# Optimization experiments

Measured on AMD Instinct MI355X. Metric: run time of the kernel, lower is better.

Reference implementation:

```python
import jax, jax.numpy as jnp
import numpy as np

B, N, T, F, H = 64, 307, 64, 3, 64
LN_EPS = 1e-5


def _layernorm(h, g, b):
    mu = h.mean(-1, keepdims=True)
    var = ((h - mu) ** 2).mean(-1, keepdims=True)
    return (h - mu) * jax.lax.rsqrt(var + LN_EPS) * g + b


def setup_inputs() -> dict:
    key = jax.random.key(0)
    ks = jax.random.split(key, 14)
    x_seq = jax.random.normal(ks[0], (B, N, T, F), dtype=jnp.float32)
    obs_mask = (jax.random.uniform(ks[1], (B, N, 1, 1)) < 0.7).astype(jnp.float32)
    # symmetric degree-normalized Gaussian-kernel adjacency [N, N]
    d = jax.random.uniform(ks[2], (N, N))
    adj = jnp.exp(-(d ** 2))
    adj = 0.5 * (adj + adj.T)
    deg = adj.sum(1)
    dinv = jnp.where(deg > 0, deg ** -0.5, 0.0)
    A = (adj * dinv[:, None] * dinv[None, :]).astype(jnp.float32)

    def lin(k, fan_in, shape):
        return (jax.random.normal(k, shape, dtype=jnp.float32) / np.sqrt(fan_in)).astype(jnp.float32)

    return {
        "x_seq": x_seq, "obs_mask": obs_mask, "A": A,
        "W_enc": lin(ks[3], F, (F, H)), "b_enc": jnp.zeros((H,), jnp.float32),
        "W_gc1": lin(ks[4], H, (H, H)),
        "W_gc2": lin(ks[5], H, (H, H)),
        "ln_g": jnp.ones((H,), jnp.float32), "ln_b": jnp.zeros((H,), jnp.float32),
        "W_obs": lin(ks[6], F, (F, H)), "b_obs": jnp.zeros((H,), jnp.float32),
        "W_gate": lin(ks[7], 2 * H, (2 * H, H)), "b_gate": jnp.zeros((H,), jnp.float32),
        "W_dec": lin(ks[8], H, (H, 1)), "b_dec": jnp.zeros((1,), jnp.float32),
    }


def reference(x_seq, obs_mask, A, W_enc, b_enc, W_gc1, W_gc2, ln_g, ln_b,
              W_obs, b_obs, W_gate, b_gate, W_dec, b_dec):
    mask = obs_mask[:, :, 0, :]                      # [B, N, 1]
    z0 = x_seq[:, :, 0, :] @ W_enc + b_enc           # [B, N, H]
    xs = jnp.moveaxis(x_seq[:, :, 1:, :], 2, 0)      # [T-1, B, N, F]

    def step(z, x_new):
        pred = z @ W_dec + b_dec                     # decoder before update
        # Euler step: z + ode_func(z), ode_func(x) = x + LN(tanh(gc2(tanh(gc1(x)))))
        h = jnp.tanh(jnp.einsum('nm,bmd->bnd', A, z) @ W_gc1)
        h = jnp.tanh(jnp.einsum('nm,bmd->bnd', A, h) @ W_gc2)
        delta = _layernorm(h, ln_g, ln_b)
        z = z + (z + delta)
        # gated assimilation of the new observation
        z_obs = x_new @ W_obs + b_obs
        gate = jax.nn.sigmoid(jnp.concatenate([z, z_obs], axis=-1) @ W_gate + b_gate)
        z = z + gate * (z_obs - z) * mask
        return z, pred

    z_final, preds = jax.lax.scan(step, z0, xs)      # preds: [T-1, B, N, 1]
    pred_last = z_final @ W_dec + b_dec
    preds = jnp.concatenate([preds, pred_last[None]], axis=0)  # [T, B, N, 1]
    return jnp.moveaxis(preds, 0, 2)                 # [B, N, T, 1]
```

## Files before the change

### kernel.cpp

```cpp
#include <hip/hip_runtime.h>

typedef unsigned short u16;
typedef __attribute__((ext_vector_type(8))) short short8;
typedef __attribute__((ext_vector_type(4))) float f32x4;
typedef __attribute__((ext_vector_type(4))) int i32x4;
typedef __attribute__((ext_vector_type(4))) unsigned short u16x4;

#define NN 307
#define NP 320
#define TT 64
#define LDP 76
#define LWS 68
#define LNEPS 1e-5f

__device__ __forceinline__ u16 f2bf(float f) {
  union { float f; unsigned u; } v; v.f = f;
  unsigned r = (v.u + 0x7FFFu + ((v.u >> 16) & 1u)) >> 16;
  return (u16)r;
}
__device__ __forceinline__ float bf2f(u16 h) {
  union { unsigned u; float f; } v; v.u = ((unsigned)h) << 16;
  return v.f;
}
__device__ __forceinline__ void split3(float v, u16 &h, u16 &m, u16 &l) {
  h = f2bf(v);
  float r1 = v - bf2f(h);
  m = f2bf(r1);
  float r2 = r1 - bf2f(m);
  l = f2bf(r2);
}

#define MFMA(a, b, c) __builtin_amdgcn_mfma_f32_16x16x32_bf16((a), (b), (c), 0, 0, 0)

__device__ __forceinline__ void gemm_block(
    const u16* __restrict__ A_hi, const u16* __restrict__ A_md, const u16* __restrict__ A_lo,
    const u16* __restrict__ X_hi, const u16* __restrict__ X_md, const u16* __restrict__ X_lo,
    int c0, int n0, int tid, f32x4 acc[2][2])
{
  const int w = tid >> 6, l = tid & 63, lr = l & 15, lg = l >> 4;
  const int wr = w >> 1, wc = w & 1;
  const size_t xr0 = (size_t)(c0 + wr * 32 + lr) * NP;
  const size_t xr1 = xr0 + (size_t)16 * NP;
  const size_t ar0 = (size_t)(n0 + wc * 32 + lr) * NP;
  const size_t ar1 = ar0 + (size_t)16 * NP;
  for (int kk = 0; kk < 10; ++kk) {
    const int ko = kk * 32 + lg * 8;
    short8 xh[2], xm[2], xl[2], ah[2], am[2], al[2];
    xh[0] = *(const short8*)&X_hi[xr0 + ko];
    xm[0] = *(const short8*)&X_md[xr0 + ko];
    xl[0] = *(const short8*)&X_lo[xr0 + ko];
    xh[1] = *(const short8*)&X_hi[xr1 + ko];
    xm[1] = *(const short8*)&X_md[xr1 + ko];
    xl[1] = *(const short8*)&X_lo[xr1 + ko];
    ah[0] = *(const short8*)&A_hi[ar0 + ko];
    am[0] = *(const short8*)&A_md[ar0 + ko];
    al[0] = *(const short8*)&A_lo[ar0 + ko];
    ah[1] = *(const short8*)&A_hi[ar1 + ko];
    am[1] = *(const short8*)&A_md[ar1 + ko];
    al[1] = *(const short8*)&A_lo[ar1 + ko];
#pragma unroll
    for (int fr = 0; fr < 2; ++fr) {
#pragma unroll
      for (int fc = 0; fc < 2; ++fc) {
        f32x4 a = acc[fr][fc];
        a = MFMA(xh[fr], ah[fc], a);
        a = MFMA(xh[fr], am[fc], a);
        a = MFMA(xm[fr], ah[fc], a);
        a = MFMA(xh[fr], al[fc], a);
        a = MFMA(xl[fr], ah[fc], a);
        a = MFMA(xm[fr], am[fc], a);
        acc[fr][fc] = a;
      }
    }
  }
}

__device__ __forceinline__ void store_G(f32x4 acc[2][2], float* ldsG, int tid) {
  const int w = tid >> 6, l = tid & 63, lr = l & 15, lg = l >> 4;
  const int wr = w >> 1, wc = w & 1;
#pragma unroll
  for (int fr = 0; fr < 2; ++fr) {
#pragma unroll
    for (int fc = 0; fc < 2; ++fc) {
      const int nn = wc * 32 + fc * 16 + lr;
      const int quad = (8 * wr + 4 * fr + lg) ^ (nn & 15);
      *(f32x4*)&ldsG[nn * LDP + quad * 4] = acc[fr][fc];
    }
  }
}

__device__ __forceinline__ void mat64(const float* ldsG, const float* ldsW,
                                      int nq, int dq, float o[4][4]) {
#pragma unroll
  for (int j = 0; j < 4; ++j)
#pragma unroll
    for (int c = 0; c < 4; ++c) o[j][c] = 0.f;
  for (int d4 = 0; d4 < 16; ++d4) {
    f32x4 gr[4], wv[4];
#pragma unroll
    for (int j = 0; j < 4; ++j) {
      const int nl = nq * 4 + j;
      gr[j] = *(const f32x4*)&ldsG[nl * LDP + ((d4 ^ (nl & 15)) << 2)];
    }
#pragma unroll
    for (int m = 0; m < 4; ++m)
      wv[m] = *(const f32x4*)&ldsW[(d4 * 4 + m) * LWS + dq * 4];
#pragma unroll
    for (int j = 0; j < 4; ++j) {
#pragma unroll
      for (int m = 0; m < 4; ++m) {
        const float zz = gr[j][m];
#pragma unroll
        for (int c = 0; c < 4; ++c) o[j][c] += zz * wv[m][c];
      }
    }
  }
}

__device__ __forceinline__ void stage_W(const float* __restrict__ W, float* ldsW, int tid) {
  const int d = tid >> 2, ch = (tid & 3) << 4;
#pragma unroll
  for (int j = 0; j < 16; ++j)
    ldsW[d * LWS + ch + j] = W[d * 64 + ch + j];
}

__global__ __launch_bounds__(256) void k_prep(
    const float* __restrict__ A, const float* __restrict__ W_obs,
    const float* __restrict__ b_obs, const float* __restrict__ W_gate,
    u16* __restrict__ A_hi, u16* __restrict__ A_md, u16* __restrict__ A_lo,
    float* __restrict__ Wf, float* __restrict__ bfold)
{
  if (blockIdx.x < 400) {
    const int e = blockIdx.x * 256 + threadIdx.x;
    const int r = e / NP, c = e - r * NP;
    const float a = (r < NN && c < NN) ? A[r * NN + c] : 0.f;
    u16 h, m, l;
    split3(a, h, m, l);
    A_hi[e] = h; A_md[e] = m; A_lo[e] = l;
  } else if (threadIdx.x < 64) {
    const int dp = threadIdx.x;
    float s0 = 0.f, s1 = 0.f, s2 = 0.f, sb = 0.f;
    for (int d = 0; d < 64; ++d) {
      const float wg = W_gate[(64 + d) * 64 + dp];
      s0 += W_obs[d] * wg;
      s1 += W_obs[64 + d] * wg;
      s2 += W_obs[128 + d] * wg;
      sb += b_obs[d] * wg;
    }
    Wf[dp] = s0; Wf[64 + dp] = s1; Wf[128 + dp] = s2; bfold[dp] = sb;
  }
}

__global__ __launch_bounds__(256) void k_init(
    const float* __restrict__ x_seq, const float* __restrict__ W_enc,
    const float* __restrict__ b_enc, const float* __restrict__ W_dec,
    const float* __restrict__ b_dec,
    float* __restrict__ zf,
    u16* __restrict__ Z_hi, u16* __restrict__ Z_md, u16* __restrict__ Z_lo,
    float* __restrict__ out)
{
  const int b = blockIdx.x, n0 = blockIdx.y * 64;
  const int tid = threadIdx.x;
  __shared__ float xs[256], we[192], be[64], wd[64];
  __shared__ float ldsR[16 * 64];
  if (tid < 64) {
    const int n = n0 + tid;
    float x0 = 0.f, x1 = 0.f, x2 = 0.f;
    if (n < NN) {
      const size_t xo = ((size_t)(b * NN + n) * TT + 0) * 3;
      x0 = x_seq[xo]; x1 = x_seq[xo + 1]; x2 = x_seq[xo + 2];
    }
    xs[tid * 4] = x0; xs[tid * 4 + 1] = x1; xs[tid * 4 + 2] = x2; xs[tid * 4 + 3] = 0.f;
    be[tid] = b_enc[tid]; wd[tid] = W_dec[tid];
  } else {
    const int e = tid - 64;
    if (e < 192) we[e] = W_enc[e];
  }
  __syncthreads();
  const int nq = tid & 15, dq = tid >> 4;
  float zn[4][4];
  float p[4] = {0.f, 0.f, 0.f, 0.f};
#pragma unroll
  for (int j = 0; j < 4; ++j) {
    const int nl = nq * 4 + j;
    const bool v = (n0 + nl) < NN;
    const float x0 = xs[nl * 4], x1 = xs[nl * 4 + 1], x2 = xs[nl * 4 + 2];
#pragma unroll
    for (int c = 0; c < 4; ++c) {
      const int d = dq * 4 + c;
      float z = x0 * we[d] + x1 * we[64 + d] + x2 * we[128 + d] + be[d];
      z = v ? z : 0.f;
      zn[j][c] = z;
      p[j] += z * wd[d];
    }
  }
#pragma unroll
  for (int c = 0; c < 4; ++c) {
    const int d = dq * 4 + c;
    const size_t off = (size_t)(b * 64 + d) * NP + n0 + nq * 4;
    f32x4 vf = { zn[0][c], zn[1][c], zn[2][c], zn[3][c] };
    *(f32x4*)&zf[off] = vf;
    u16x4 vh, vm, vl;
#pragma unroll
    for (int j = 0; j < 4; ++j) {
      u16 hh, mm2, ll;
      split3(zn[j][c], hh, mm2, ll);
      vh[j] = hh; vm[j] = mm2; vl[j] = ll;
    }
    *(u16x4*)&Z_hi[off] = vh;
    *(u16x4*)&Z_md[off] = vm;
    *(u16x4*)&Z_lo[off] = vl;
  }
#pragma unroll
  for (int j = 0; j < 4; ++j) ldsR[dq * 64 + nq * 4 + j] = p[j];
  __syncthreads();
  if (tid < 64) {
    const int n = n0 + tid;
    if (n < NN) {
      float s = 0.f;
#pragma unroll
      for (int q = 0; q < 16; ++q) s += ldsR[q * 64 + tid];
      out[(size_t)(b * NN + n) * TT + 0] = s + b_dec[0];
    }
  }
}

__global__ __launch_bounds__(256) void k_step1(
    const u16* __restrict__ A_hi, const u16* __restrict__ A_md, const u16* __restrict__ A_lo,
    const u16* __restrict__ X_hi, const u16* __restrict__ X_md, const u16* __restrict__ X_lo,
    const float* __restrict__ W_gc1,
    u16* __restrict__ O_hi, u16* __restrict__ O_md, u16* __restrict__ O_lo)
{
  const int b = blockIdx.x, n0 = blockIdx.y * 64, c0 = b * 64;
  const int tid = threadIdx.x;
  __shared__ __align__(16) float ldsG[64 * LDP];
  __shared__ __align__(16) float ldsW[64 * LWS];
  stage_W(W_gc1, ldsW, tid);
  f32x4 acc[2][2];
  acc[0][0] = 0.f; acc[0][1] = 0.f; acc[1][0] = 0.f; acc[1][1] = 0.f;
  gemm_block(A_hi, A_md, A_lo, X_hi, X_md, X_lo, c0, n0, tid, acc);
  store_G(acc, ldsG, tid);
  __syncthreads();
  const int nq = tid & 15, dq = tid >> 4;
  float mx[4][4];
  mat64(ldsG, ldsW, nq, dq, mx);
#pragma unroll
  for (int c = 0; c < 4; ++c) {
    u16x4 vh, vm, vl;
#pragma unroll
    for (int j = 0; j < 4; ++j) {
      const float v = tanhf(mx[j][c]);
      u16 hh, mm2, ll;
      split3(v, hh, mm2, ll);
      vh[j] = hh; vm[j] = mm2; vl[j] = ll;
    }
    const size_t off = (size_t)(c0 + dq * 4 + c) * NP + n0 + nq * 4;
    *(u16x4*)&O_hi[off] = vh;
    *(u16x4*)&O_md[off] = vm;
    *(u16x4*)&O_lo[off] = vl;
  }
}

__global__ __launch_bounds__(256) void k_step2(
    const u16* __restrict__ A_hi, const u16* __restrict__ A_md, const u16* __restrict__ A_lo,
    const u16* __restrict__ X_hi, const u16* __restrict__ X_md, const u16* __restrict__ X_lo,
    const float* __restrict__ W_gc2,
    const float* __restrict__ x_seq, const float* __restrict__ obs_mask,
    const float* __restrict__ W_gate, const float* __restrict__ b_gate,
    const float* __restrict__ ln_g, const float* __restrict__ ln_b,
    const float* __restrict__ W_obs, const float* __restrict__ b_obs,
    const float* __restrict__ Wf, const float* __restrict__ bfold,
    const float* __restrict__ W_dec, const float* __restrict__ b_dec,
    float* __restrict__ zf,
    u16* __restrict__ Z_hi, u16* __restrict__ Z_md, u16* __restrict__ Z_lo,
    float* __restrict__ out, int t)
{
  const int b = blockIdx.x, n0 = blockIdx.y * 64, c0 = b * 64;
  const int tid = threadIdx.x;
  __shared__ __align__(16) float ldsG[64 * LDP];
  __shared__ __align__(16) float ldsW[64 * LWS];
  __shared__ __align__(16) float ldsWg[64 * LWS];
  __shared__ float ldsR[16 * 64];
  __shared__ float ldsMu[64], ldsRs[64];
  __shared__ float sLng[64], sLnb[64], sWd[64], sBg[64], sBo[64], sBf[64], sMask[64];
  __shared__ float sWo[192], sWfl[192], sXv[256];

  stage_W(W_gc2, ldsW, tid);
  stage_W(W_gate, ldsWg, tid);
  if (tid < 64) {
    sLng[tid] = ln_g[tid]; sLnb[tid] = ln_b[tid]; sWd[tid] = W_dec[tid];
    sBg[tid] = b_gate[tid]; sBo[tid] = b_obs[tid]; sBf[tid] = bfold[tid];
    const int n = n0 + tid;
    sMask[tid] = (n < NN) ? obs_mask[b * NN + n] : 0.f;
    float x0 = 0.f, x1 = 0.f, x2 = 0.f;
    if (n < NN) {
      const size_t xo = ((size_t)(b * NN + n) * TT + (t + 1)) * 3;
      x0 = x_seq[xo]; x1 = x_seq[xo + 1]; x2 = x_seq[xo + 2];
    }
    sXv[tid * 4] = x0; sXv[tid * 4 + 1] = x1; sXv[tid * 4 + 2] = x2; sXv[tid * 4 + 3] = 0.f;
  } else {
    const int e = tid - 64;
    if (e < 192) { sWo[e] = W_obs[e]; sWfl[e] = Wf[e]; }
  }

  f32x4 acc[2][2];
  acc[0][0] = 0.f; acc[0][1] = 0.f; acc[1][0] = 0.f; acc[1][1] = 0.f;
  gemm_block(A_hi, A_md, A_lo, X_hi, X_md, X_lo, c0, n0, tid, acc);
  store_G(acc, ldsG, tid);
  __syncthreads();

  const int nq = tid & 15, dq = tid >> 4;
  float mx[4][4];
  mat64(ldsG, ldsW, nq, dq, mx);
  float h2[4][4];
#pragma unroll
  for (int j = 0; j < 4; ++j)
#pragma unroll
    for (int c = 0; c < 4; ++c) h2[j][c] = tanhf(mx[j][c]);

#pragma unroll
  for (int j = 0; j < 4; ++j)
    ldsR[dq * 64 + nq * 4 + j] = h2[j][0] + h2[j][1] + h2[j][2] + h2[j][3];
  __syncthreads();
  if (tid < 64) {
    float s = 0.f;
#pragma unroll
    for (int q = 0; q < 16; ++q) s += ldsR[q * 64 + tid];
    ldsMu[tid] = s * (1.f / 64.f);
  }
  __syncthreads();
#pragma unroll
  for (int j = 0; j < 4; ++j) {
    const float mu = ldsMu[nq * 4 + j];
    float qq = 0.f;
#pragma unroll
    for (int c = 0; c < 4; ++c) { const float dd = h2[j][c] - mu; qq += dd * dd; }
    ldsR[dq * 64 + nq * 4 + j] = qq;
  }
  __syncthreads();
  if (tid < 64) {
    float s = 0.f;
#pragma unroll
    for (int q = 0; q < 16; ++q) s += ldsR[q * 64 + tid];
    ldsRs[tid] = rsqrtf(s * (1.f / 64.f) + LNEPS);
  }
  __syncthreads();

  f32x4 zoldv[4];
#pragma unroll
  for (int c = 0; c < 4; ++c)
    zoldv[c] = *(const f32x4*)&zf[(size_t)(c0 + dq * 4 + c) * NP + n0 + nq * 4];
  float zpr[4][4];
#pragma unroll
  for (int j = 0; j < 4; ++j) {
    const int nl = nq * 4 + j;
    const float mu = ldsMu[nl], rs = ldsRs[nl];
#pragma unroll
    for (int c = 0; c < 4; ++c) {
      const int dpp = dq * 4 + c;
      const float delta = (h2[j][c] - mu) * rs * sLng[dpp] + sLnb[dpp];
      zpr[j][c] = 2.f * zoldv[c][j] + delta;
    }
    f32x4 zrow = { zpr[j][0], zpr[j][1], zpr[j][2], zpr[j][3] };
    *(f32x4*)&ldsG[nl * LDP + ((dq ^ (nl & 15)) << 2)] = zrow;
  }
  __syncthreads();

  float ps[4][4];
  mat64(ldsG, ldsWg, nq, dq, ps);

  float znew[4][4];
  float p[4] = {0.f, 0.f, 0.f, 0.f};
#pragma unroll
  for (int j = 0; j < 4; ++j) {
    const int nl = nq * 4 + j;
    const bool valid = (n0 + nl) < NN;
    const float x0 = sXv[nl * 4], x1 = sXv[nl * 4 + 1], x2 = sXv[nl * 4 + 2];
    const float mk = sMask[nl];
#pragma unroll
    for (int c = 0; c < 4; ++c) {
      const int dpp = dq * 4 + c;
      const float presig = ps[j][c] + sBg[dpp] + sBf[dpp]
          + x0 * sWfl[dpp] + x1 * sWfl[64 + dpp] + x2 * sWfl[128 + dpp];
      const float gate = 1.f / (1.f + expf(-presig));
      const float zobs = x0 * sWo[dpp] + x1 * sWo[64 + dpp] + x2 * sWo[128 + dpp] + sBo[dpp];
      float zn2 = zpr[j][c] + gate * (zobs - zpr[j][c]) * mk;
      zn2 = valid ? zn2 : 0.f;
      znew[j][c] = zn2;
      p[j] += zn2 * sWd[dpp];
    }
  }
#pragma unroll
  for (int c = 0; c < 4; ++c) {
    const size_t off = (size_t)(c0 + dq * 4 + c) * NP + n0 + nq * 4;
    f32x4 vf = { znew[0][c], znew[1][c], znew[2][c], znew[3][c] };
    *(f32x4*)&zf[off] = vf;
    u16x4 vh, vm, vl;
#pragma unroll
    for (int j = 0; j < 4; ++j) {
      u16 hh, mm2, ll;
      split3(znew[j][c], hh, mm2, ll);
      vh[j] = hh; vm[j] = mm2; vl[j] = ll;
    }
    *(u16x4*)&Z_hi[off] = vh;
    *(u16x4*)&Z_md[off] = vm;
    *(u16x4*)&Z_lo[off] = vl;
  }
#pragma unroll
  for (int j = 0; j < 4; ++j) ldsR[dq * 64 + nq * 4 + j] = p[j];
  __syncthreads();
  if (tid < 64) {
    const int n = n0 + tid;
    if (n < NN) {
      float s = 0.f;
#pragma unroll
      for (int q = 0; q < 16; ++q) s += ldsR[q * 64 + tid];
      out[(size_t)(b * NN + n) * TT + (t + 1)] = s + b_dec[0];
    }
  }
}

extern "C" void kernel_launch(void* const* d_in, const int* in_sizes, int n_in,
                              void* d_out, int out_size, void* d_ws, size_t ws_size,
                              hipStream_t stream) {
  const float* x_seq  = (const float*)d_in[0];
  const float* obs    = (const float*)d_in[1];
  const float* A      = (const float*)d_in[2];
  const float* W_enc  = (const float*)d_in[3];
  const float* b_enc  = (const float*)d_in[4];
  const float* W_gc1  = (const float*)d_in[5];
  const float* W_gc2  = (const float*)d_in[6];
  const float* ln_g   = (const float*)d_in[7];
  const float* ln_b   = (const float*)d_in[8];
  const float* W_obs  = (const float*)d_in[9];
  const float* b_obs  = (const float*)d_in[10];
  const float* W_gate = (const float*)d_in[11];
  const float* b_gate = (const float*)d_in[12];
  const float* W_dec  = (const float*)d_in[13];
  const float* b_dec  = (const float*)d_in[14];
  float* out = (float*)d_out;

  char* p = (char*)d_ws;
  u16* A_hi = (u16*)p; p += (size_t)NP * NP * 2;
  u16* A_md = (u16*)p; p += (size_t)NP * NP * 2;
  u16* A_lo = (u16*)p; p += (size_t)NP * NP * 2;
  u16* z_hi = (u16*)p; p += (size_t)4096 * NP * 2;
  u16* z_md = (u16*)p; p += (size_t)4096 * NP * 2;
  u16* z_lo = (u16*)p; p += (size_t)4096 * NP * 2;
  u16* h_hi = (u16*)p; p += (size_t)4096 * NP * 2;
  u16* h_md = (u16*)p; p += (size_t)4096 * NP * 2;
  u16* h_lo = (u16*)p; p += (size_t)4096 * NP * 2;
  float* zf = (float*)p; p += (size_t)4096 * NP * 4;
  float* Wf = (float*)p; p += 256 * 4;
  float* bfold = (float*)p; p += 64 * 4;

  dim3 grid(64, 5);
  k_prep<<<401, 256, 0, stream>>>(A, W_obs, b_obs, W_gate, A_hi, A_md, A_lo, Wf, bfold);
  k_init<<<grid, 256, 0, stream>>>(x_seq, W_enc, b_enc, W_dec, b_dec,
                                   zf, z_hi, z_md, z_lo, out);
  for (int t = 0; t < 63; ++t) {
    k_step1<<<grid, 256, 0, stream>>>(A_hi, A_md, A_lo, z_hi, z_md, z_lo, W_gc1,
                                      h_hi, h_md, h_lo);
    k_step2<<<grid, 256, 0, stream>>>(A_hi, A_md, A_lo, h_hi, h_md, h_lo, W_gc2,
                                      x_seq, obs, W_gate, b_gate, ln_g, ln_b,
                                      W_obs, b_obs, Wf, bfold, W_dec, b_dec,
                                      zf, z_hi, z_md, z_lo, out, t);
  }
  (void)in_sizes; (void)n_in; (void)out_size; (void)ws_size;
}
```

Baseline: 12.76 ms.

## Fuse all time steps into one persistent kernel per batch element

Replaces the 127 per-step kernel launches (init plus two per step) with one persistent kernel of 64 blocks, one per batch, that loops over all 63 time steps internally. It keeps the fp32 state z in registers instead of a global buffer, and uses wave shuffles instead of LDS reductions for layernorm and decoder sums. This removes launch overhead and the global round-trips of z. The cost is that only 64 blocks occupy the GPU, far fewer than the CU count, so each block now carries a full 320x64 GEMM per stage. The H and Z split buffers still pass through global memory between stages, and their new per-element scalar stores are uncoalesced.

```diff
diff --git a/kernel.cpp b/kernel.cpp
--- a/kernel.cpp
+++ b/kernel.cpp
@@ -3,14 +3,12 @@
 typedef unsigned short u16;
 typedef __attribute__((ext_vector_type(8))) short short8;
 typedef __attribute__((ext_vector_type(4))) float f32x4;
-typedef __attribute__((ext_vector_type(4))) int i32x4;
-typedef __attribute__((ext_vector_type(4))) unsigned short u16x4;
 
 #define NN 307
 #define NP 320
 #define TT 64
-#define LDP 76
-#define LWS 68
+#define NB 64
+#define LDP 68
 #define LNEPS 1e-5f
 
 __device__ __forceinline__ u16 f2bf(float f) {
@@ -31,98 +29,6 @@
 }
 
 #define MFMA(a, b, c) __builtin_amdgcn_mfma_f32_16x16x32_bf16((a), (b), (c), 0, 0, 0)
-
-__device__ __forceinline__ void gemm_block(
-    const u16* __restrict__ A_hi, const u16* __restrict__ A_md, const u16* __restrict__ A_lo,
-    const u16* __restrict__ X_hi, const u16* __restrict__ X_md, const u16* __restrict__ X_lo,
-    int c0, int n0, int tid, f32x4 acc[2][2])
-{
-  const int w = tid >> 6, l = tid & 63, lr = l & 15, lg = l >> 4;
-  const int wr = w >> 1, wc = w & 1;
-  const size_t xr0 = (size_t)(c0 + wr * 32 + lr) * NP;
-  const size_t xr1 = xr0 + (size_t)16 * NP;
-  const size_t ar0 = (size_t)(n0 + wc * 32 + lr) * NP;
-  const size_t ar1 = ar0 + (size_t)16 * NP;
-  for (int kk = 0; kk < 10; ++kk) {
-    const int ko = kk * 32 + lg * 8;
-    short8 xh[2], xm[2], xl[2], ah[2], am[2], al[2];
-    xh[0] = *(const short8*)&X_hi[xr0 + ko];
-    xm[0] = *(const short8*)&X_md[xr0 + ko];
-    xl[0] = *(const short8*)&X_lo[xr0 + ko];
-    xh[1] = *(const short8*)&X_hi[xr1 + ko];
-    xm[1] = *(const short8*)&X_md[xr1 + ko];
-    xl[1] = *(const short8*)&X_lo[xr1 + ko];
-    ah[0] = *(const short8*)&A_hi[ar0 + ko];
-    am[0] = *(const short8*)&A_md[ar0 + ko];
-    al[0] = *(const short8*)&A_lo[ar0 + ko];
-    ah[1] = *(const short8*)&A_hi[ar1 + ko];
-    am[1] = *(const short8*)&A_md[ar1 + ko];
-    al[1] = *(const short8*)&A_lo[ar1 + ko];
-#pragma unroll
-    for (int fr = 0; fr < 2; ++fr) {
-#pragma unroll
-      for (int fc = 0; fc < 2; ++fc) {
-        f32x4 a = acc[fr][fc];
-        a = MFMA(xh[fr], ah[fc], a);
-        a = MFMA(xh[fr], am[fc], a);
-        a = MFMA(xm[fr], ah[fc], a);
-        a = MFMA(xh[fr], al[fc], a);
-        a = MFMA(xl[fr], ah[fc], a);
-        a = MFMA(xm[fr], am[fc], a);
-        acc[fr][fc] = a;
-      }
-    }
-  }
-}
-
-__device__ __forceinline__ void store_G(f32x4 acc[2][2], float* ldsG, int tid) {
-  const int w = tid >> 6, l = tid & 63, lr = l & 15, lg = l >> 4;
-  const int wr = w >> 1, wc = w & 1;
-#pragma unroll
-  for (int fr = 0; fr < 2; ++fr) {
-#pragma unroll
-    for (int fc = 0; fc < 2; ++fc) {
-      const int nn = wc * 32 + fc * 16 + lr;
-      const int quad = (8 * wr + 4 * fr + lg) ^ (nn & 15);
-      *(f32x4*)&ldsG[nn * LDP + quad * 4] = acc[fr][fc];
-    }
-  }
-}
-
-__device__ __forceinline__ void mat64(const float* ldsG, const float* ldsW,
-                                      int nq, int dq, float o[4][4]) {
-#pragma unroll
-  for (int j = 0; j < 4; ++j)
-#pragma unroll
-    for (int c = 0; c < 4; ++c) o[j][c] = 0.f;
-  for (int d4 = 0; d4 < 16; ++d4) {
-    f32x4 gr[4], wv[4];
-#pragma unroll
-    for (int j = 0; j < 4; ++j) {
-      const int nl = nq * 4 + j;
-      gr[j] = *(const f32x4*)&ldsG[nl * LDP + ((d4 ^ (nl & 15)) << 2)];
-    }
-#pragma unroll
-    for (int m = 0; m < 4; ++m)
-      wv[m] = *(const f32x4*)&ldsW[(d4 * 4 + m) * LWS + dq * 4];
-#pragma unroll
-    for (int j = 0; j < 4; ++j) {
-#pragma unroll
-      for (int m = 0; m < 4; ++m) {
-        const float zz = gr[j][m];
-#pragma unroll
-        for (int c = 0; c < 4; ++c) o[j][c] += zz * wv[m][c];
-      }
-    }
-  }
-}
-
-__device__ __forceinline__ void stage_W(const float* __restrict__ W, float* ldsW, int tid) {
-  const int d = tid >> 2, ch = (tid & 3) << 4;
-#pragma unroll
-  for (int j = 0; j < 16; ++j)
-    ldsW[d * LWS + ch + j] = W[d * 64 + ch + j];
-}
 
 __global__ __launch_bounds__(256) void k_prep(
     const float* __restrict__ A, const float* __restrict__ W_obs,
@@ -151,272 +57,241 @@
   }
 }
 
-__global__ __launch_bounds__(256) void k_init(
-    const float* __restrict__ x_seq, const float* __restrict__ W_enc,
-    const float* __restrict__ b_enc, const float* __restrict__ W_dec,
-    const float* __restrict__ b_dec,
-    float* __restrict__ zf,
+__device__ __forceinline__ void gemm_stage(
+    const u16* __restrict__ Xh, const u16* __restrict__ Xm, const u16* __restrict__ Xl,
+    const u16* __restrict__ Ah, const u16* __restrict__ Am, const u16* __restrict__ Al,
+    int b, int cr, int g160, int lr, int lg, float* ldsG)
+{
+  const size_t xbase = (size_t)(b * 64 + cr * 16 + lr) * NP;
+  f32x4 acc[10];
+#pragma unroll
+  for (int i = 0; i < 10; ++i) acc[i] = (f32x4){0.f, 0.f, 0.f, 0.f};
+  unsigned abase[10];
+#pragma unroll
+  for (int i = 0; i < 10; ++i) abase[i] = (unsigned)((g160 + i * 16 + lr) * NP);
+
+  for (int kk = 0; kk < 10; ++kk) {
+    const int ko = kk * 32 + lg * 8;
+    const short8 xh = *(const short8*)&Xh[xbase + ko];
+    const short8 xm = *(const short8*)&Xm[xbase + ko];
+    const short8 xl = *(const short8*)&Xl[xbase + ko];
+#pragma unroll
+    for (int i = 0; i < 10; ++i) {
+      const short8 ah = *(const short8*)&Ah[abase[i] + ko];
+      const short8 am = *(const short8*)&Am[abase[i] + ko];
+      const short8 al = *(const short8*)&Al[abase[i] + ko];
+      f32x4 a = acc[i];
+      a = MFMA(xh, ah, a);
+      a = MFMA(xh, am, a);
+      a = MFMA(xm, ah, a);
+      a = MFMA(xh, al, a);
+      a = MFMA(xl, ah, a);
+      a = MFMA(xm, am, a);
+      acc[i] = a;
+    }
+  }
+#pragma unroll
+  for (int i = 0; i < 10; ++i) {
+    const int n = g160 + i * 16 + lr;
+    const int q = cr * 4 + lg;
+    *(f32x4*)&ldsG[n * LDP + ((q ^ (n & 15)) << 2)] = acc[i];
+  }
+}
+
+__device__ __forceinline__ void mat64b(const float* __restrict__ ldsG,
+                                       const float* __restrict__ ldsW,
+                                       int nset, int dq, float o[10][4])
+{
+#pragma unroll
+  for (int i = 0; i < 10; ++i)
+#pragma unroll
+    for (int c = 0; c < 4; ++c) o[i][c] = 0.f;
+  const int nq15 = nset & 15;
+  for (int d4 = 0; d4 < 16; ++d4) {
+    f32x4 wv[4];
+#pragma unroll
+    for (int m = 0; m < 4; ++m)
+      wv[m] = *(const f32x4*)&ldsW[(d4 * 4 + m) * 64 + dq * 4];
+#pragma unroll
+    for (int i = 0; i < 10; ++i) {
+      const f32x4 gr = *(const f32x4*)&ldsG[(nset + 32 * i) * LDP + ((d4 ^ nq15) << 2)];
+#pragma unroll
+      for (int m = 0; m < 4; ++m) {
+        const float g = gr[m];
+#pragma unroll
+        for (int c = 0; c < 4; ++c) o[i][c] += g * wv[m][c];
+      }
+    }
+  }
+}
+
+__global__ __launch_bounds__(512, 1) void k_main(
+    const float* __restrict__ x_seq, const float* __restrict__ obs_mask,
+    const float* __restrict__ W_enc, const float* __restrict__ b_enc,
+    const float* __restrict__ ln_g, const float* __restrict__ ln_b,
+    const float* __restrict__ W_obs, const float* __restrict__ b_obs,
+    const float* __restrict__ W_gate, const float* __restrict__ b_gate,
+    const float* __restrict__ W_dec, const float* __restrict__ b_dec,
+    const float* __restrict__ W_gc1, const float* __restrict__ W_gc2,
+    const float* __restrict__ Wf, const float* __restrict__ bfold,
+    const u16* __restrict__ A_hi, const u16* __restrict__ A_md, const u16* __restrict__ A_lo,
     u16* __restrict__ Z_hi, u16* __restrict__ Z_md, u16* __restrict__ Z_lo,
+    u16* __restrict__ H_hi, u16* __restrict__ H_md, u16* __restrict__ H_lo,
     float* __restrict__ out)
 {
-  const int b = blockIdx.x, n0 = blockIdx.y * 64;
+  const int b = blockIdx.x;
   const int tid = threadIdx.x;
-  __shared__ float xs[256], we[192], be[64], wd[64];
-  __shared__ float ldsR[16 * 64];
-  if (tid < 64) {
-    const int n = n0 + tid;
+  const int w = tid >> 6, l = tid & 63, lr = l & 15, lg = l >> 4;
+  const int dq = tid & 15, nset = tid >> 4;
+  const int cr = w & 3, g160 = (w >> 2) * 160;
+
+  __shared__ __align__(16) float ldsG[NP * LDP];
+  __shared__ __align__(16) float ldsW1[64 * 64];
+  __shared__ __align__(16) float ldsW2[64 * 64];
+  __shared__ __align__(16) float ldsWg[64 * 64];
+  __shared__ float sXv[NP * 4];
+  __shared__ float sMask[NP];
+  __shared__ float sWo[192], sWfl[192], sWe[192];
+  __shared__ float sBe[64], sLng[64], sLnb[64], sWd[64], sBg[64], sBo[64], sBf[64];
+
+#pragma unroll
+  for (int j = 0; j < 8; ++j) {
+    ldsW1[tid * 8 + j] = W_gc1[tid * 8 + j];
+    ldsW2[tid * 8 + j] = W_gc2[tid * 8 + j];
+    ldsWg[tid * 8 + j] = W_gate[tid * 8 + j];
+  }
+  if (tid < 192) { sWo[tid] = W_obs[tid]; sWfl[tid] = Wf[tid]; sWe[tid] = W_enc[tid]; }
+  else if (tid < 256) {
+    const int d = tid - 192;
+    sBe[d] = b_enc[d]; sLng[d] = ln_g[d]; sLnb[d] = ln_b[d]; sWd[d] = W_dec[d];
+    sBg[d] = b_gate[d]; sBo[d] = b_obs[d]; sBf[d] = bfold[d];
+  }
+  if (tid < NP) {
+    const int n = tid;
+    sMask[n] = (n < NN) ? obs_mask[b * NN + n] : 0.f;
     float x0 = 0.f, x1 = 0.f, x2 = 0.f;
     if (n < NN) {
-      const size_t xo = ((size_t)(b * NN + n) * TT + 0) * 3;
+      const size_t xo = ((size_t)(b * NN + n) * TT) * 3;
       x0 = x_seq[xo]; x1 = x_seq[xo + 1]; x2 = x_seq[xo + 2];
     }
-    xs[tid * 4] = x0; xs[tid * 4 + 1] = x1; xs[tid * 4 + 2] = x2; xs[tid * 4 + 3] = 0.f;
-    be[tid] = b_enc[tid]; wd[tid] = W_dec[tid];
-  } else {
-    const int e = tid - 64;
-    if (e < 192) we[e] = W_enc[e];
-  }
+    sXv[n * 4] = x0; sXv[n * 4 + 1] = x1; sXv[n * 4 + 2] = x2; sXv[n * 4 + 3] = 0.f;
+  }
+  const float bdec = b_dec[0];
   __syncthreads();
-  const int nq = tid & 15, dq = tid >> 4;
-  float zn[4][4];
-  float p[4] = {0.f, 0.f, 0.f, 0.f};
-#pragma unroll
-  for (int j = 0; j < 4; ++j) {
-    const int nl = nq * 4 + j;
-    const bool v = (n0 + nl) < NN;
-    const float x0 = xs[nl * 4], x1 = xs[nl * 4 + 1], x2 = xs[nl * 4 + 2];
-#pragma unroll
-    for (int c = 0; c < 4; ++c) {
-      const int d = dq * 4 + c;
-      float z = x0 * we[d] + x1 * we[64 + d] + x2 * we[128 + d] + be[d];
-      z = v ? z : 0.f;
-      zn[j][c] = z;
-      p[j] += z * wd[d];
-    }
-  }
-#pragma unroll
-  for (int c = 0; c < 4; ++c) {
-    const int d = dq * 4 + c;
-    const size_t off = (size_t)(b * 64 + d) * NP + n0 + nq * 4;
-    f32x4 vf = { zn[0][c], zn[1][c], zn[2][c], zn[3][c] };
-    *(f32x4*)&zf[off] = vf;
-    u16x4 vh, vm, vl;
-#pragma unroll
-    for (int j = 0; j < 4; ++j) {
-      u16 hh, mm2, ll;
-      split3(zn[j][c], hh, mm2, ll);
-      vh[j] = hh; vm[j] = mm2; vl[j] = ll;
-    }
-    *(u16x4*)&Z_hi[off] = vh;
-    *(u16x4*)&Z_md[off] = vm;
-    *(u16x4*)&Z_lo[off] = vl;
-  }
-#pragma unroll
-  for (int j = 0; j < 4; ++j) ldsR[dq * 64 + nq * 4 + j] = p[j];
-  __syncthreads();
-  if (tid < 64) {
-    const int n = n0 + tid;
-    if (n < NN) {
-      float s = 0.f;
-#pragma unroll
-      for (int q = 0; q < 16; ++q) s += ldsR[q * 64 + tid];
-      out[(size_t)(b * NN + n) * TT + 0] = s + b_dec[0];
-    }
-  }
-}
-
-__global__ __launch_bounds__(256) void k_step1(
-    const u16* __restrict__ A_hi, const u16* __restrict__ A_md, const u16* __restrict__ A_lo,
-    const u16* __restrict__ X_hi, const u16* __restrict__ X_md, const u16* __restrict__ X_lo,
-    const float* __restrict__ W_gc1,
-    u16* __restrict__ O_hi, u16* __restrict__ O_md, u16* __restrict__ O_lo)
-{
-  const int b = blockIdx.x, n0 = blockIdx.y * 64, c0 = b * 64;
-  const int tid = threadIdx.x;
-  __shared__ __align__(16) float ldsG[64 * LDP];
-  __shared__ __align__(16) float ldsW[64 * LWS];
-  stage_W(W_gc1, ldsW, tid);
-  f32x4 acc[2][2];
-  acc[0][0] = 0.f; acc[0][1] = 0.f; acc[1][0] = 0.f; acc[1][1] = 0.f;
-  gemm_block(A_hi, A_md, A_lo, X_hi, X_md, X_lo, c0, n0, tid, acc);
-  store_G(acc, ldsG, tid);
-  __syncthreads();
-  const int nq = tid & 15, dq = tid >> 4;
-  float mx[4][4];
-  mat64(ldsG, ldsW, nq, dq, mx);
-#pragma unroll
-  for (int c = 0; c < 4; ++c) {
-    u16x4 vh, vm, vl;
-#pragma unroll
-    for (int j = 0; j < 4; ++j) {
-      const float v = tanhf(mx[j][c]);
-      u16 hh, mm2, ll;
-      split3(v, hh, mm2, ll);
-      vh[j] = hh; vm[j] = mm2; vl[j] = ll;
-    }
-    const size_t off = (size_t)(c0 + dq * 4 + c) * NP + n0 + nq * 4;
-    *(u16x4*)&O_hi[off] = vh;
-    *(u16x4*)&O_md[off] = vm;
-    *(u16x4*)&O_lo[off] = vl;
-  }
-}
-
-__global__ __launch_bounds__(256) void k_step2(
-    const u16* __restrict__ A_hi, const u16* __restrict__ A_md, const u16* __restrict__ A_lo,
-    const u16* __restrict__ X_hi, const u16* __restrict__ X_md, const u16* __restrict__ X_lo,
-    const float* __restrict__ W_gc2,
-    const float* __restrict__ x_seq, const float* __restrict__ obs_mask,
-    const float* __restrict__ W_gate, const float* __restrict__ b_gate,
-    const float* __restrict__ ln_g, const float* __restrict__ ln_b,
-    const float* __restrict__ W_obs, const float* __restrict__ b_obs,
-    const float* __restrict__ Wf, const float* __restrict__ bfold,
-    const float* __restrict__ W_dec, const float* __restrict__ b_dec,
-    float* __restrict__ zf,
-    u16* __restrict__ Z_hi, u16* __restrict__ Z_md, u16* __restrict__ Z_lo,
-    float* __restrict__ out, int t)
-{
-  const int b = blockIdx.x, n0 = blockIdx.y * 64, c0 = b * 64;
-  const int tid = threadIdx.x;
-  __shared__ __align__(16) float ldsG[64 * LDP];
-  __shared__ __align__(16) float ldsW[64 * LWS];
-  __shared__ __align__(16) float ldsWg[64 * LWS];
-  __shared__ float ldsR[16 * 64];
-  __shared__ float ldsMu[64], ldsRs[64];
-  __shared__ float sLng[64], sLnb[64], sWd[64], sBg[64], sBo[64], sBf[64], sMask[64];
-  __shared__ float sWo[192], sWfl[192], sXv[256];
-
-  stage_W(W_gc2, ldsW, tid);
-  stage_W(W_gate, ldsWg, tid);
-  if (tid < 64) {
-    sLng[tid] = ln_g[tid]; sLnb[tid] = ln_b[tid]; sWd[tid] = W_dec[tid];
-    sBg[tid] = b_gate[tid]; sBo[tid] = b_obs[tid]; sBf[tid] = bfold[tid];
-    const int n = n0 + tid;
-    sMask[tid] = (n < NN) ? obs_mask[b * NN + n] : 0.f;
-    float x0 = 0.f, x1 = 0.f, x2 = 0.f;
-    if (n < NN) {
-      const size_t xo = ((size_t)(b * NN + n) * TT + (t + 1)) * 3;
-      x0 = x_seq[xo]; x1 = x_seq[xo + 1]; x2 = x_seq[xo + 2];
-    }
-    sXv[tid * 4] = x0; sXv[tid * 4 + 1] = x1; sXv[tid * 4 + 2] = x2; sXv[tid * 4 + 3] = 0.f;
-  } else {
-    const int e = tid - 64;
-    if (e < 192) { sWo[e] = W_obs[e]; sWfl[e] = Wf[e]; }
-  }
-
-  f32x4 acc[2][2];
-  acc[0][0] = 0.f; acc[0][1] = 0.f; acc[1][0] = 0.f; acc[1][1] = 0.f;
-  gemm_block(A_hi, A_md, A_lo, X_hi, X_md, X_lo, c0, n0, tid, acc);
-  store_G(acc, ldsG, tid);
-  __syncthreads();
-
-  const int nq = tid & 15, dq = tid >> 4;
-  float mx[4][4];
-  mat64(ldsG, ldsW, nq, dq, mx);
-  float h2[4][4];
-#pragma unroll
-  for (int j = 0; j < 4; ++j)
-#pragma unroll
-    for (int c = 0; c < 4; ++c) h2[j][c] = tanhf(mx[j][c]);
-
-#pragma unroll
-  for (int j = 0; j < 4; ++j)
-    ldsR[dq * 64 + nq * 4 + j] = h2[j][0] + h2[j][1] + h2[j][2] + h2[j][3];
-  __syncthreads();
-  if (tid < 64) {
-    float s = 0.f;
-#pragma unroll
-    for (int q = 0; q < 16; ++q) s += ldsR[q * 64 + tid];
-    ldsMu[tid] = s * (1.f / 64.f);
-  }
-  __syncthreads();
-#pragma unroll
-  for (int j = 0; j < 4; ++j) {
-    const float mu = ldsMu[nq * 4 + j];
-    float qq = 0.f;
-#pragma unroll
-    for (int c = 0; c < 4; ++c) { const float dd = h2[j][c] - mu; qq += dd * dd; }
-    ldsR[dq * 64 + nq * 4 + j] = qq;
-  }
-  __syncthreads();
-  if (tid < 64) {
-    float s = 0.f;
-#pragma unroll
-    for (int q = 0; q < 16; ++q) s += ldsR[q * 64 + tid];
-    ldsRs[tid] = rsqrtf(s * (1.f / 64.f) + LNEPS);
-  }
-  __syncthreads();
-
-  f32x4 zoldv[4];
-#pragma unroll
-  for (int c = 0; c < 4; ++c)
-    zoldv[c] = *(const f32x4*)&zf[(size_t)(c0 + dq * 4 + c) * NP + n0 + nq * 4];
-  float zpr[4][4];
-#pragma unroll
-  for (int j = 0; j < 4; ++j) {
-    const int nl = nq * 4 + j;
-    const float mu = ldsMu[nl], rs = ldsRs[nl];
+
+  float zf[10][4];
+#pragma unroll
+  for (int i = 0; i < 10; ++i) {
+    const int n = nset + 32 * i;
+    const bool valid = n < NN;
+    const float x0 = sXv[n * 4], x1 = sXv[n * 4 + 1], x2 = sXv[n * 4 + 2];
+    float p = 0.f;
 #pragma unroll
     for (int c = 0; c < 4; ++c) {
       const int dpp = dq * 4 + c;
-      const float delta = (h2[j][c] - mu) * rs * sLng[dpp] + sLnb[dpp];
-      zpr[j][c] = 2.f * zoldv[c][j] + delta;
-    }
-    f32x4 zrow = { zpr[j][0], zpr[j][1], zpr[j][2], zpr[j][3] };
-    *(f32x4*)&ldsG[nl * LDP + ((dq ^ (nl & 15)) << 2)] = zrow;
+      float z = x0 * sWe[dpp] + x1 * sWe[64 + dpp] + x2 * sWe[128 + dpp] + sBe[dpp];
+      z = valid ? z : 0.f;
+      zf[i][c] = z;
+      u16 hh, mm, ll; split3(z, hh, mm, ll);
+      const size_t off = (size_t)(b * 64 + dpp) * NP + n;
+      Z_hi[off] = hh; Z_md[off] = mm; Z_lo[off] = ll;
+      p += z * sWd[dpp];
+    }
+#pragma unroll
+    for (int m = 1; m < 16; m <<= 1) p += __shfl_xor(p, m, 64);
+    if (dq == 0 && valid) out[(size_t)(b * NN + n) * TT] = p + bdec;
   }
   __syncthreads();
 
-  float ps[4][4];
-  mat64(ldsG, ldsWg, nq, dq, ps);
-
-  float znew[4][4];
-  float p[4] = {0.f, 0.f, 0.f, 0.f};
-#pragma unroll
-  for (int j = 0; j < 4; ++j) {
-    const int nl = nq * 4 + j;
-    const bool valid = (n0 + nl) < NN;
-    const float x0 = sXv[nl * 4], x1 = sXv[nl * 4 + 1], x2 = sXv[nl * 4 + 2];
-    const float mk = sMask[nl];
-#pragma unroll
-    for (int c = 0; c < 4; ++c) {
-      const int dpp = dq * 4 + c;
-      const float presig = ps[j][c] + sBg[dpp] + sBf[dpp]
-          + x0 * sWfl[dpp] + x1 * sWfl[64 + dpp] + x2 * sWfl[128 + dpp];
-      const float gate = 1.f / (1.f + expf(-presig));
-      const float zobs = x0 * sWo[dpp] + x1 * sWo[64 + dpp] + x2 * sWo[128 + dpp] + sBo[dpp];
-      float zn2 = zpr[j][c] + gate * (zobs - zpr[j][c]) * mk;
-      zn2 = valid ? zn2 : 0.f;
-      znew[j][c] = zn2;
-      p[j] += zn2 * sWd[dpp];
-    }
-  }
-#pragma unroll
-  for (int c = 0; c < 4; ++c) {
-    const size_t off = (size_t)(c0 + dq * 4 + c) * NP + n0 + nq * 4;
-    f32x4 vf = { znew[0][c], znew[1][c], znew[2][c], znew[3][c] };
-    *(f32x4*)&zf[off] = vf;
-    u16x4 vh, vm, vl;
-#pragma unroll
-    for (int j = 0; j < 4; ++j) {
-      u16 hh, mm2, ll;
-      split3(znew[j][c], hh, mm2, ll);
-      vh[j] = hh; vm[j] = mm2; vl[j] = ll;
-    }
-    *(u16x4*)&Z_hi[off] = vh;
-    *(u16x4*)&Z_md[off] = vm;
-    *(u16x4*)&Z_lo[off] = vl;
-  }
-#pragma unroll
-  for (int j = 0; j < 4; ++j) ldsR[dq * 64 + nq * 4 + j] = p[j];
-  __syncthreads();
-  if (tid < 64) {
-    const int n = n0 + tid;
-    if (n < NN) {
-      float s = 0.f;
-#pragma unroll
-      for (int q = 0; q < 16; ++q) s += ldsR[q * 64 + tid];
-      out[(size_t)(b * NN + n) * TT + (t + 1)] = s + b_dec[0];
-    }
+  for (int t = 0; t < 63; ++t) {
+    float px0 = 0.f, px1 = 0.f, px2 = 0.f;
+    if (tid < NN) {
+      const size_t xo = ((size_t)(b * NN + tid) * TT + (t + 1)) * 3;
+      px0 = x_seq[xo]; px1 = x_seq[xo + 1]; px2 = x_seq[xo + 2];
+    }
+    gemm_stage(Z_hi, Z_md, Z_lo, A_hi, A_md, A_lo, b, cr, g160, lr, lg, ldsG);
+    if (tid < NP) {
+      sXv[tid * 4] = px0; sXv[tid * 4 + 1] = px1; sXv[tid * 4 + 2] = px2;
+    }
+    __syncthreads();
+    {
+      float o[10][4];
+      mat64b(ldsG, ldsW1, nset, dq, o);
+#pragma unroll
+      for (int i = 0; i < 10; ++i) {
+        const int n = nset + 32 * i;
+#pragma unroll
+        for (int c = 0; c < 4; ++c) {
+          const float h = tanhf(o[i][c]);
+          u16 hh, mm, ll; split3(h, hh, mm, ll);
+          const size_t off = (size_t)(b * 64 + dq * 4 + c) * NP + n;
+          H_hi[off] = hh; H_md[off] = mm; H_lo[off] = ll;
+        }
+      }
+    }
+    __syncthreads();
+
+    gemm_stage(H_hi, H_md, H_lo, A_hi, A_md, A_lo, b, cr, g160, lr, lg, ldsG);
+    __syncthreads();
+    {
+      float o[10][4];
+      mat64b(ldsG, ldsW2, nset, dq, o);
+      float zp[10][4];
+      const int nq15 = nset & 15;
+#pragma unroll
+      for (int i = 0; i < 10; ++i) {
+        float h2[4];
+#pragma unroll
+        for (int c = 0; c < 4; ++c) h2[c] = tanhf(o[i][c]);
+        float s = h2[0] + h2[1] + h2[2] + h2[3];
+#pragma unroll
+        for (int m = 1; m < 16; m <<= 1) s += __shfl_xor(s, m, 64);
+        const float mu = s * (1.f / 64.f);
+        float q = 0.f;
+#pragma unroll
+        for (int c = 0; c < 4; ++c) { const float d0 = h2[c] - mu; q += d0 * d0; }
+#pragma unroll
+        for (int m = 1; m < 16; m <<= 1) q += __shfl_xor(q, m, 64);
+        const float rs = rsqrtf(q * (1.f / 64.f) + LNEPS);
+#pragma unroll
+        for (int c = 0; c < 4; ++c) {
+          const int dpp = dq * 4 + c;
+          const float delta = (h2[c] - mu) * rs * sLng[dpp] + sLnb[dpp];
+          zp[i][c] = 2.f * zf[i][c] + delta;
+        }
+        f32x4 zrow = { zp[i][0], zp[i][1], zp[i][2], zp[i][3] };
+        *(f32x4*)&ldsG[(nset + 32 * i) * LDP + ((dq ^ nq15) << 2)] = zrow;
+      }
+      float ps[10][4];
+      mat64b(ldsG, ldsWg, nset, dq, ps);
+#pragma unroll
+      for (int i = 0; i < 10; ++i) {
+        const int n = nset + 32 * i;
+        const bool valid = n < NN;
+        const float x0 = sXv[n * 4], x1 = sXv[n * 4 + 1], x2 = sXv[n * 4 + 2];
+        const float mk = sMask[n];
+        float p = 0.f;
+#pragma unroll
+        for (int c = 0; c < 4; ++c) {
+          const int dpp = dq * 4 + c;
+          const float presig = ps[i][c] + sBg[dpp] + sBf[dpp]
+              + x0 * sWfl[dpp] + x1 * sWfl[64 + dpp] + x2 * sWfl[128 + dpp];
+          const float gate = 1.f / (1.f + expf(-presig));
+          const float zobs = x0 * sWo[dpp] + x1 * sWo[64 + dpp] + x2 * sWo[128 + dpp] + sBo[dpp];
+          float zn = zp[i][c] + gate * (zobs - zp[i][c]) * mk;
+          zn = valid ? zn : 0.f;
+          zf[i][c] = zn;
+          u16 hh, mm, ll; split3(zn, hh, mm, ll);
+          const size_t off = (size_t)(b * 64 + dpp) * NP + n;
+          Z_hi[off] = hh; Z_md[off] = mm; Z_lo[off] = ll;
+          p += zn * sWd[dpp];
+        }
+#pragma unroll
+        for (int m = 1; m < 16; m <<= 1) p += __shfl_xor(p, m, 64);
+        if (dq == 0 && valid) out[(size_t)(b * NN + n) * TT + (t + 1)] = p + bdec;
+      }
+    }
+    __syncthreads();
   }
 }
 
@@ -450,21 +325,14 @@
   u16* h_hi = (u16*)p; p += (size_t)4096 * NP * 2;
   u16* h_md = (u16*)p; p += (size_t)4096 * NP * 2;
   u16* h_lo = (u16*)p; p += (size_t)4096 * NP * 2;
-  float* zf = (float*)p; p += (size_t)4096 * NP * 4;
   float* Wf = (float*)p; p += 256 * 4;
   float* bfold = (float*)p; p += 64 * 4;
 
-  dim3 grid(64, 5);
   k_prep<<<401, 256, 0, stream>>>(A, W_obs, b_obs, W_gate, A_hi, A_md, A_lo, Wf, bfold);
-  k_init<<<grid, 256, 0, stream>>>(x_seq, W_enc, b_enc, W_dec, b_dec,
-                                   zf, z_hi, z_md, z_lo, out);
-  for (int t = 0; t < 63; ++t) {
-    k_step1<<<grid, 256, 0, stream>>>(A_hi, A_md, A_lo, z_hi, z_md, z_lo, W_gc1,
-                                      h_hi, h_md, h_lo);
-    k_step2<<<grid, 256, 0, stream>>>(A_hi, A_md, A_lo, h_hi, h_md, h_lo, W_gc2,
-                                      x_seq, obs, W_gate, b_gate, ln_g, ln_b,
-                                      W_obs, b_obs, Wf, bfold, W_dec, b_dec,
-                                      zf, z_hi, z_md, z_lo, out, t);
-  }
+  k_main<<<NB, 512, 0, stream>>>(x_seq, obs, W_enc, b_enc, ln_g, ln_b,
+                                 W_obs, b_obs, W_gate, b_gate, W_dec, b_dec,
+                                 W_gc1, W_gc2, Wf, bfold,
+                                 A_hi, A_md, A_lo,
+                                 z_hi, z_md, z_lo, h_hi, h_md, h_lo, out);
   (void)in_sizes; (void)n_in; (void)out_size; (void)ws_size;
 }
```

After: 14.58 ms. 14.3% more time.
